# Kernel optimization log

Measured on AMD Instinct MI355X. Metric: run time of the kernel, lower is better.

The kernel has to match this reference:

```python
import jax, jax.numpy as jnp
import numpy as np

N_EMBED = 1024
N_HEADS = 16
HEAD_SIZE = N_EMBED // N_HEADS
BLOCK_SIZE = 256
LN_EPS = 1e-5


def _layernorm(x, g, b):
    mu = jnp.mean(x, axis=-1, keepdims=True)
    var = jnp.var(x, axis=-1, keepdims=True)
    return (x - mu) * jax.lax.rsqrt(var + LN_EPS) * g + b


def setup_inputs() -> dict:
    key = jax.random.key(0)
    ks = jax.random.split(key, 12)
    B, T, C, H, D = 64, 256, N_EMBED, N_HEADS, HEAD_SIZE
    s = lambda fan_in: 1.0 / np.sqrt(fan_in)
    return {
        "x": jax.random.normal(ks[0], (B, T, C), jnp.float32),
        # per-head Q/K/V projections (bias=False in torch), stacked over heads
        "Wq": jax.random.uniform(ks[1], (H, C, D), jnp.float32, -s(C), s(C)),
        "Wk": jax.random.uniform(ks[2], (H, C, D), jnp.float32, -s(C), s(C)),
        "Wv": jax.random.uniform(ks[3], (H, C, D), jnp.float32, -s(C), s(C)),
        "Wproj": jax.random.uniform(ks[4], (C, C), jnp.float32, -s(C), s(C)),
        "bproj": jax.random.uniform(ks[5], (C,), jnp.float32, -s(C), s(C)),
        "W1": jax.random.uniform(ks[6], (C, 4 * C), jnp.float32, -s(C), s(C)),
        "b1": jax.random.uniform(ks[7], (4 * C,), jnp.float32, -s(C), s(C)),
        "W2": jax.random.uniform(ks[8], (4 * C, C), jnp.float32, -s(4 * C), s(4 * C)),
        "b2": jax.random.uniform(ks[9], (C,), jnp.float32, -s(4 * C), s(4 * C)),
        "ln1_g": jnp.ones((C,), jnp.float32),
        "ln1_b": jnp.zeros((C,), jnp.float32),
        "ln2_g": jnp.ones((C,), jnp.float32),
        "ln2_b": jnp.zeros((C,), jnp.float32),
    }


def reference(x, Wq, Wk, Wv, Wproj, bproj, W1, b1, W2, b2, ln1_g, ln1_b, ln2_g, ln2_b):
    B, T, C = x.shape
    # --- self-attention sub-block ---
    h = _layernorm(x, ln1_g, ln1_b)
    q = jnp.einsum("btc,hcd->bhtd", h, Wq)
    k = jnp.einsum("btc,hcd->bhtd", h, Wk)
    v = jnp.einsum("btc,hcd->bhtd", h, Wv)
    # NOTE: original scales by C**-0.5 with C = n_embed (full dim), not head_size
    scores = jnp.einsum("bhtd,bhsd->bhts", q, k) * (C ** -0.5)
    causal = jnp.tril(jnp.ones((T, T), bool))
    scores = jnp.where(causal, scores, -jnp.inf)
    wei = jax.nn.softmax(scores, axis=-1)
    attn = jnp.einsum("bhts,bhsd->bhtd", wei, v)  # [B,H,T,D]
    attn = attn.transpose(0, 2, 1, 3).reshape(B, T, C)  # concat heads
    x = x + attn @ Wproj + bproj
    # --- feed-forward sub-block ---
    h2 = _layernorm(x, ln2_g, ln2_b)
    ffn = jax.nn.relu(h2 @ W1 + b1) @ W2 + b2
    return x + ffn
```

## Files before the change

### kernel.cpp

```cpp
#include <hip/hip_runtime.h>
#include <stdint.h>

using u16 = unsigned short;
using u32 = unsigned int;

typedef __attribute__((ext_vector_type(8))) short s16x8;
typedef __attribute__((ext_vector_type(4))) float f32x4;

__device__ __forceinline__ float bf2f(u16 u) { u32 t = (u32)u << 16; float f; __builtin_memcpy(&f, &t, 4); return f; }
__device__ __forceinline__ u16 f2bf(float f) {
  u32 u; __builtin_memcpy(&u, &f, 4);
  return (u16)((u + 0x7fffu + ((u >> 16) & 1u)) >> 16);
}

__device__ __forceinline__ void gload_lds16(const void* g, void* l) {
  __builtin_amdgcn_global_load_lds((const __attribute__((address_space(1))) void*)g,
                                   (__attribute__((address_space(3))) void*)l, 16, 0, 0);
}

__global__ __launch_bounds__(256)
void transpose_pack(const float* __restrict__ in, u16* __restrict__ out,
                    int R, int Cc, long in_bs, long out_bs)
{
  __shared__ float tile[32][33];
  in  += (size_t)blockIdx.z * in_bs;
  out += (size_t)blockIdx.z * out_bs;
  const int r0 = blockIdx.x * 32, c0 = blockIdx.y * 32;
  const int tx = threadIdx.x & 31, ty = threadIdx.x >> 5;
#pragma unroll
  for (int i = 0; i < 4; ++i) {
    int r = ty + i * 8;
    tile[r][tx] = in[(size_t)(r0 + r) * Cc + c0 + tx];
  }
  __syncthreads();
#pragma unroll
  for (int i = 0; i < 4; ++i) {
    int c = ty + i * 8;
    out[(size_t)(c0 + c) * R + r0 + tx] = f2bf(tile[tx][c]);
  }
}

template <int IN>
__global__ __launch_bounds__(256)
void ln_to_bf16(const void* __restrict__ xv, const float* __restrict__ g,
                const float* __restrict__ bta, u16* __restrict__ out)
{
  const int row = blockIdx.x, tid = threadIdx.x;
  float4 v;
  if constexpr (IN == 0) {
    v = ((const float4*)((const float*)xv + (size_t)row * 1024))[tid];
  } else {
    uint2 u = ((const uint2*)((const u16*)xv + (size_t)row * 1024))[tid];
    v.x = bf2f((u16)(u.x & 0xffff)); v.y = bf2f((u16)(u.x >> 16));
    v.z = bf2f((u16)(u.y & 0xffff)); v.w = bf2f((u16)(u.y >> 16));
  }
  float s  = v.x + v.y + v.z + v.w;
  float ss = v.x * v.x + v.y * v.y + v.z * v.z + v.w * v.w;
#pragma unroll
  for (int m = 1; m < 64; m <<= 1) {
    s  += __shfl_xor(s, m);
    ss += __shfl_xor(ss, m);
  }
  __shared__ float red[8];
  const int wave = tid >> 6, lane = tid & 63;
  if (lane == 0) { red[wave] = s; red[4 + wave] = ss; }
  __syncthreads();
  s  = red[0] + red[1] + red[2] + red[3];
  ss = red[4] + red[5] + red[6] + red[7];
  const float mu  = s * (1.f / 1024.f);
  const float var = ss * (1.f / 1024.f) - mu * mu;
  const float rs  = rsqrtf(var + 1e-5f);
  const float4 gg = ((const float4*)g)[tid];
  const float4 bb = ((const float4*)bta)[tid];
  u32 w0 = (u32)f2bf((v.x - mu) * rs * gg.x + bb.x) | ((u32)f2bf((v.y - mu) * rs * gg.y + bb.y) << 16);
  u32 w1 = (u32)f2bf((v.z - mu) * rs * gg.z + bb.z) | ((u32)f2bf((v.w - mu) * rs * gg.w + bb.w) << 16);
  u32* outp = (u32*)(out + (size_t)row * 1024 + tid * 4);
  outp[0] = w0; outp[1] = w1;
}

#define DSR(d, a, o) asm volatile("ds_read_b128 %0, %1 offset:" o : "=v"(d) : "v"(a))
#define ISSUE12(aR, bR) \
  DSR(bv0, bR, "0"); DSR(bv1, bR, "2048"); DSR(bv2, bR, "4096"); DSR(bv3, bR, "6144"); \
  DSR(av0, aR, "0"); DSR(av1, aR, "2048"); DSR(av2, aR, "4096"); DSR(av3, aR, "6144"); \
  DSR(av4, aR, "8192"); DSR(av5, aR, "10240"); DSR(av6, aR, "12288"); DSR(av7, aR, "14336")
#define MM(m, n) acc[m][n] = __builtin_amdgcn_mfma_f32_16x16x32_bf16(av##m, bv##n, acc[m][n], 0, 0, 0)
#define RUNG(m, cnt) \
  asm volatile("s_waitcnt lgkmcnt(" #cnt ")" ::: "memory"); \
  __builtin_amdgcn_sched_barrier(0); \
  MM(m, 0); MM(m, 1); MM(m, 2); MM(m, 3)
#define LADDER() \
  RUNG(0, 7); RUNG(1, 6); RUNG(2, 5); RUNG(3, 4); \
  RUNG(4, 3); RUNG(5, 2); RUNG(6, 1); RUNG(7, 0)

template <int EPI>
__device__ __forceinline__ void gemm_epilogue(f32x4 (&acc)[8][4], void* Cv, const float* bias,
                                              const void* resid, int N, int bm, int bn,
                                              int wr, int wc, int r, int kg)
{
#pragma unroll
  for (int m = 0; m < 8; ++m) {
#pragma unroll
    for (int n = 0; n < 4; ++n) {
#pragma unroll
      for (int j = 0; j < 4; ++j) {
        int row = bm * 256 + wr * 128 + m * 16 + kg * 4 + j;
        int col = bn * 256 + wc * 64 + n * 16 + r;
        size_t idx = (size_t)row * N + col;
        float v = acc[m][n][j];
        if constexpr (EPI == 0) {
          ((u16*)Cv)[idx] = f2bf(v);
        } else if constexpr (EPI == 1) {
          ((u16*)Cv)[idx] = f2bf(v + bias[col] + ((const float*)resid)[idx]);
        } else if constexpr (EPI == 2) {
          ((u16*)Cv)[idx] = f2bf(fmaxf(v + bias[col], 0.f));
        } else {
          ((float*)Cv)[idx] = v + bias[col] + bf2f(((const u16*)resid)[idx]);
        }
      }
    }
  }
}

template <int EPI>
__global__ __launch_bounds__(512, 2)
void gemm8p(const u16* __restrict__ A, const u16* __restrict__ B, void* __restrict__ Cv,
            const float* __restrict__ bias, const void* __restrict__ resid,
            int M, int N, int K, int CM, int CN, int XN)
{
  __shared__ u16 lds[65536];
  const int NT = K >> 6;
  const int tid = threadIdx.x;
  const int lane = tid & 63, wv = tid >> 6;
  const int wr = wv >> 2, wc = wv & 3;
  const int r = lane & 15, kg = lane >> 4;

  const int bid = blockIdx.x;
  const int x = bid & 7, i = bid >> 3;
  const int bm = (x / XN) * CM + i / CN;
  const int bn = (x % XN) * CN + i % CN;

  const u16* Ab = A + (size_t)bm * 256 * K;
  const u16* Bb = B + (size_t)bn * 256 * K;

  const u32 ldsb = (u32)(uintptr_t)lds;
  const u32 segb = (u32)((kg ^ (r >> 1)) << 4);
  const u32 abase = ldsb + (u32)((wr * 128 + r) * 128) + segb;
  const u32 bbase = ldsb + 65536u + (u32)((wc * 64 + r) * 128) + segb;

  f32x4 acc[8][4];
#pragma unroll
  for (int m = 0; m < 8; ++m)
#pragma unroll
    for (int n = 0; n < 4; ++n) acc[m][n] = f32x4{0.f, 0.f, 0.f, 0.f};

  auto stage = [&](const u16* src, int u, int h, int base_u16) {
#pragma unroll
    for (int jj = 0; jj < 2; ++jj) {
      int ci = jj * 512 + tid;
      int rl = ci >> 3;
      int sseg = (ci & 7) ^ ((rl >> 1) & 7);
      gload_lds16(src + (size_t)(h * 128 + rl) * K + u * 64 + sseg * 8,
                  &lds[base_u16 + h * 8192 + ci * 8]);
    }
  };

  stage(Ab, 0, 0, 0);      stage(Ab, 0, 1, 0);
  stage(Bb, 0, 0, 32768);  stage(Bb, 0, 1, 32768);
  asm volatile("s_waitcnt vmcnt(0)" ::: "memory");
  __builtin_amdgcn_s_barrier();

  for (int t = 0; t < NT; ++t) {
    const int buf = t & 1;
    const bool s1 = (t + 1) < NT;
    const int nb = (buf ^ 1) * 16384;
    const u32 aA0 = abase + (u32)(buf * 32768);
    const u32 aB0 = bbase + (u32)(buf * 32768);

    if (s1) {
      stage(Ab, t + 1, 0, nb);           stage(Ab, t + 1, 1, nb);
      stage(Bb, t + 1, 0, 32768 + nb);   stage(Bb, t + 1, 1, 32768 + nb);
    }
    __builtin_amdgcn_sched_barrier(0);
    __builtin_amdgcn_s_setprio(1);
    {
      s16x8 av0, av1, av2, av3, av4, av5, av6, av7, bv0, bv1, bv2, bv3;
      ISSUE12(aA0, aB0);
      LADDER();
    }
    {
      s16x8 av0, av1, av2, av3, av4, av5, av6, av7, bv0, bv1, bv2, bv3;
      ISSUE12(aA0 ^ 64u, aB0 ^ 64u);
      LADDER();
    }
    __builtin_amdgcn_s_setprio(0);
    __builtin_amdgcn_sched_barrier(0);
    asm volatile("s_waitcnt vmcnt(0)" ::: "memory");
    __builtin_amdgcn_s_barrier();
  }
  gemm_epilogue<EPI>(acc, Cv, bias, resid, N, bm, bn, wr, wc, r, kg);
}

template <int EPI>
__global__ __launch_bounds__(512, 2)
void gemm1b(const u16* __restrict__ A, const u16* __restrict__ B, void* __restrict__ Cv,
            const float* __restrict__ bias, const void* __restrict__ resid,
            int M, int N, int K, int CM, int CN, int XN)
{
  __shared__ u16 lds[32768];
  const int NT = K >> 6;
  const int tid = threadIdx.x;
  const int lane = tid & 63, wv = tid >> 6;
  const int wr = wv >> 2, wc = wv & 3;
  const int r = lane & 15, kg = lane >> 4;

  const int bid = blockIdx.x;
  const int x = bid & 7, i = bid >> 3;
  const int bm = (x / XN) * CM + i / CN;
  const int bn = (x % XN) * CN + i % CN;

  const u16* Ab = A + (size_t)bm * 256 * K;
  const u16* Bb = B + (size_t)bn * 256 * K;

  const u32 ldsb = (u32)(uintptr_t)lds;
  const u32 segb = (u32)((kg ^ (r >> 1)) << 4);
  const u32 aA0 = ldsb + (u32)((wr * 128 + r) * 128) + segb;
  const u32 aB0 = ldsb + 32768u + (u32)((wc * 64 + r) * 128) + segb;

  f32x4 acc[8][4];
#pragma unroll
  for (int m = 0; m < 8; ++m)
#pragma unroll
    for (int n = 0; n < 4; ++n) acc[m][n] = f32x4{0.f, 0.f, 0.f, 0.f};

  auto stage = [&](const u16* src, int u, int h, int base_u16) {
#pragma unroll
    for (int jj = 0; jj < 2; ++jj) {
      int ci = jj * 512 + tid;
      int rl = ci >> 3;
      int sseg = (ci & 7) ^ ((rl >> 1) & 7);
      gload_lds16(src + (size_t)(h * 128 + rl) * K + u * 64 + sseg * 8,
                  &lds[base_u16 + h * 8192 + ci * 8]);
    }
  };

  stage(Ab, 0, 0, 0);      stage(Ab, 0, 1, 0);
  stage(Bb, 0, 0, 16384);  stage(Bb, 0, 1, 16384);
  asm volatile("s_waitcnt vmcnt(0)" ::: "memory");
  __builtin_amdgcn_s_barrier();

  for (int t = 0; t < NT; ++t) {
    const bool s1 = (t + 1) < NT;
    __builtin_amdgcn_s_setprio(1);
    {
      s16x8 av0, av1, av2, av3, av4, av5, av6, av7, bv0, bv1, bv2, bv3;
      ISSUE12(aA0, aB0);
      LADDER();
    }
    {
      s16x8 av0, av1, av2, av3, av4, av5, av6, av7, bv0, bv1, bv2, bv3;
      ISSUE12(aA0 ^ 64u, aB0 ^ 64u);
      RUNG(0, 7); RUNG(1, 6); RUNG(2, 5); RUNG(3, 4);
      asm volatile("s_waitcnt lgkmcnt(0)" ::: "memory");
      __builtin_amdgcn_sched_barrier(0);
      __builtin_amdgcn_s_setprio(0);
      __builtin_amdgcn_s_barrier();
      __builtin_amdgcn_sched_barrier(0);
      if (s1) {
        stage(Ab, t + 1, 0, 0);      stage(Ab, t + 1, 1, 0);
        stage(Bb, t + 1, 0, 16384);  stage(Bb, t + 1, 1, 16384);
      }
      __builtin_amdgcn_sched_barrier(0);
      __builtin_amdgcn_s_setprio(1);
      MM(4, 0); MM(4, 1); MM(4, 2); MM(4, 3);
      MM(5, 0); MM(5, 1); MM(5, 2); MM(5, 3);
      MM(6, 0); MM(6, 1); MM(6, 2); MM(6, 3);
      MM(7, 0); MM(7, 1); MM(7, 2); MM(7, 3);
    }
    __builtin_amdgcn_s_setprio(0);
    __builtin_amdgcn_sched_barrier(0);
    asm volatile("s_waitcnt vmcnt(0)" ::: "memory");
    __builtin_amdgcn_s_barrier();
  }
  gemm_epilogue<EPI>(acc, Cv, bias, resid, N, bm, bn, wr, wc, r, kg);
}

#undef DSR
#undef ISSUE12
#undef MM
#undef RUNG
#undef LADDER

__global__ __launch_bounds__(256)
void attn_mfma(const u16* __restrict__ qkv, u16* __restrict__ outc)
{
  const int bh = blockIdx.x, b = bh >> 4, h = bh & 15;
  const int tid = threadIdx.x;
  const int lane = tid & 63, w = tid >> 6;
  const int r = lane & 15, kg = lane >> 4;

  __shared__ u16 Ks[64 * 64];
  __shared__ u16 Vt[64 * 72];
  __shared__ u16 P[4][64 * 72];

  const u16* qbase = qkv + (size_t)(b * 256) * 3072 + h * 64;

  s16x8 qf[4][2];
#pragma unroll
  for (int m = 0; m < 4; ++m)
#pragma unroll
    for (int ks = 0; ks < 2; ++ks)
      qf[m][ks] = *(const s16x8*)(qbase + (size_t)(w * 64 + m * 16 + r) * 3072 + ks * 32 + kg * 8);

  f32x4 of[4][4];
  float mrun[4][4], lrun[4][4];
#pragma unroll
  for (int m = 0; m < 4; ++m) {
#pragma unroll
    for (int n = 0; n < 4; ++n) of[m][n] = f32x4{0.f, 0.f, 0.f, 0.f};
#pragma unroll
    for (int j = 0; j < 4; ++j) { mrun[m][j] = -1e30f; lrun[m][j] = 0.f; }
  }

  const float cexp = 0.03125f * 1.4426950408889634f;

  for (int kt = 0; kt < 4; ++kt) {
#pragma unroll
    for (int jj = 0; jj < 2; ++jj) {
      int ci = jj * 256 + tid;
      int key = ci >> 3, seg = ci & 7;
      int sseg = seg ^ (key & 7);
      gload_lds16(qkv + (size_t)(b * 256 + kt * 64 + key) * 3072 + 1024 + h * 64 + sseg * 8,
                  &Ks[ci * 8]);
    }
    {
      int row = tid >> 2, q = tid & 3;
      const u16* vg = qkv + (size_t)(b * 256 + kt * 64 + row) * 3072 + 2048 + h * 64 + q * 16;
      union { uint4 u[2]; u16 s[16]; } vv;
      vv.u[0] = *(const uint4*)vg;
      vv.u[1] = *(const uint4*)(vg + 8);
#pragma unroll
      for (int i = 0; i < 16; ++i)
        Vt[(q * 16 + i) * 72 + row] = vv.s[i];
    }
    __syncthreads();

    if (w >= kt) {
      f32x4 s[4][4];
#pragma unroll
      for (int m = 0; m < 4; ++m)
#pragma unroll
        for (int n = 0; n < 4; ++n) s[m][n] = f32x4{0.f, 0.f, 0.f, 0.f};
#pragma unroll
      for (int ks = 0; ks < 2; ++ks) {
        s16x8 kb[4];
#pragma unroll
        for (int n = 0; n < 4; ++n) {
          int row = n * 16 + r;
          int sseg = (ks * 4 + kg) ^ (row & 7);
          kb[n] = *(const s16x8*)&Ks[row * 64 + sseg * 8];
        }
#pragma unroll
        for (int m = 0; m < 4; ++m)
#pragma unroll
          for (int n = 0; n < 4; ++n)
            s[m][n] = __builtin_amdgcn_mfma_f32_16x16x32_bf16(qf[m][ks], kb[n], s[m][n], 0, 0, 0);
      }
      if (kt == w) {
#pragma unroll
        for (int m = 0; m < 4; ++m)
#pragma unroll
          for (int n = 0; n < 4; ++n)
#pragma unroll
            for (int j = 0; j < 4; ++j)
              if (n * 16 + r > m * 16 + kg * 4 + j) s[m][n][j] = -1e30f;
      }
#pragma unroll
      for (int m = 0; m < 4; ++m) {
        float rm[4], rsc[4], ls[4];
#pragma unroll
        for (int j = 0; j < 4; ++j) {
          rm[j] = fmaxf(fmaxf(s[m][0][j], s[m][1][j]), fmaxf(s[m][2][j], s[m][3][j]));
          rm[j] = fmaxf(rm[j], __shfl_xor(rm[j], 1));
          rm[j] = fmaxf(rm[j], __shfl_xor(rm[j], 2));
          rm[j] = fmaxf(rm[j], __shfl_xor(rm[j], 4));
          rm[j] = fmaxf(rm[j], __shfl_xor(rm[j], 8));
          float mnew = fmaxf(mrun[m][j], rm[j]);
          rsc[j] = exp2f((mrun[m][j] - mnew) * cexp);
          mrun[m][j] = mnew;
          ls[j] = 0.f;
        }
#pragma unroll
        for (int n = 0; n < 4; ++n)
#pragma unroll
          for (int j = 0; j < 4; ++j) {
            float p = exp2f((s[m][n][j] - mrun[m][j]) * cexp);
            ls[j] += p;
            P[w][(m * 16 + kg * 4 + j) * 72 + n * 16 + r] = f2bf(p);
          }
#pragma unroll
        for (int j = 0; j < 4; ++j) {
          ls[j] += __shfl_xor(ls[j], 1);
          ls[j] += __shfl_xor(ls[j], 2);
          ls[j] += __shfl_xor(ls[j], 4);
          ls[j] += __shfl_xor(ls[j], 8);
          lrun[m][j] = lrun[m][j] * rsc[j] + ls[j];
        }
#pragma unroll
        for (int n = 0; n < 4; ++n)
#pragma unroll
          for (int j = 0; j < 4; ++j)
            of[m][n][j] *= rsc[j];
      }
#pragma unroll
      for (int kk = 0; kk < 2; ++kk) {
        s16x8 pa[4], vb[4];
#pragma unroll
        for (int m = 0; m < 4; ++m)
          pa[m] = *(const s16x8*)&P[w][(m * 16 + r) * 72 + kk * 32 + kg * 8];
#pragma unroll
        for (int n = 0; n < 4; ++n)
          vb[n] = *(const s16x8*)&Vt[(n * 16 + r) * 72 + kk * 32 + kg * 8];
#pragma unroll
        for (int m = 0; m < 4; ++m)
#pragma unroll
          for (int n = 0; n < 4; ++n)
            of[m][n] = __builtin_amdgcn_mfma_f32_16x16x32_bf16(pa[m], vb[n], of[m][n], 0, 0, 0);
      }
    }
    __syncthreads();
  }

#pragma unroll
  for (int m = 0; m < 4; ++m) {
    float inv[4];
#pragma unroll
    for (int j = 0; j < 4; ++j) inv[j] = 1.f / lrun[m][j];
#pragma unroll
    for (int n = 0; n < 4; ++n)
#pragma unroll
      for (int j = 0; j < 4; ++j) {
        int row = b * 256 + w * 64 + m * 16 + kg * 4 + j;
        outc[(size_t)row * 1024 + h * 64 + n * 16 + r] = f2bf(of[m][n][j] * inv[j]);
      }
  }
}

extern "C" void kernel_launch(void* const* d_in, const int* in_sizes, int n_in,
                              void* d_out, int out_size, void* d_ws, size_t ws_size,
                              hipStream_t stream) {
  (void)in_sizes; (void)n_in; (void)out_size; (void)ws_size;
  const float* x     = (const float*)d_in[0];
  const float* Wq    = (const float*)d_in[1];
  const float* Wk    = (const float*)d_in[2];
  const float* Wv    = (const float*)d_in[3];
  const float* Wproj = (const float*)d_in[4];
  const float* bproj = (const float*)d_in[5];
  const float* W1    = (const float*)d_in[6];
  const float* b1    = (const float*)d_in[7];
  const float* W2    = (const float*)d_in[8];
  const float* b2    = (const float*)d_in[9];
  const float* ln1g  = (const float*)d_in[10];
  const float* ln1b  = (const float*)d_in[11];
  const float* ln2g  = (const float*)d_in[12];
  const float* ln2b  = (const float*)d_in[13];
  float* out = (float*)d_out;

  char* ws = (char*)d_ws;
  u16*   WqkvT  = (u16*)(ws + 0);
  u16*   WprojT = (u16*)(ws + 6291456);
  u16*   W1T    = (u16*)(ws + 8388608);
  u16*   W2T    = (u16*)(ws + 16777216);
  u16*   hb     = (u16*)(ws + 25165824);
  u16*   qkvb   = (u16*)(ws + 58720256);
  u16*   x2     = (u16*)(ws + 159383552);
  u16*   h2     = (u16*)(ws + 226492416);
  u16*   ffn1   = (u16*)(ws + 25165824);
  u16*   attnout = hb;

  const int M = 16384;

  transpose_pack<<<dim3(32, 2, 16), 256, 0, stream>>>(Wq, WqkvT,           1024, 64, 65536, 65536);
  transpose_pack<<<dim3(32, 2, 16), 256, 0, stream>>>(Wk, WqkvT + 1048576, 1024, 64, 65536, 65536);
  transpose_pack<<<dim3(32, 2, 16), 256, 0, stream>>>(Wv, WqkvT + 2097152, 1024, 64, 65536, 65536);
  transpose_pack<<<dim3(32, 32, 1), 256, 0, stream>>>(Wproj, WprojT, 1024, 1024, 0, 0);
  transpose_pack<<<dim3(32, 128, 1), 256, 0, stream>>>(W1, W1T, 1024, 4096, 0, 0);
  transpose_pack<<<dim3(128, 32, 1), 256, 0, stream>>>(W2, W2T, 4096, 1024, 0, 0);

  ln_to_bf16<0><<<M, 256, 0, stream>>>(x, ln1g, ln1b, hb);

  gemm8p<0><<<768, 512, 0, stream>>>(hb, WqkvT, qkvb, nullptr, nullptr, M, 3072, 1024, 16, 6, 2);

  attn_mfma<<<1024, 256, 0, stream>>>(qkvb, attnout);

  gemm8p<1><<<256, 512, 0, stream>>>(attnout, WprojT, x2, bproj, x, M, 1024, 1024, 8, 4, 1);

  ln_to_bf16<1><<<M, 256, 0, stream>>>(x2, ln2g, ln2b, h2);

  gemm1b<2><<<1024, 512, 0, stream>>>(h2, W1T, ffn1, b1, nullptr, M, 4096, 1024, 16, 8, 2);

  gemm1b<3><<<256, 512, 0, stream>>>(ffn1, W2T, out, b2, x2, M, 1024, 4096, 8, 4, 1);
}
```

Baseline: 611.4 us.

## Shrink FFN GEMM tiles to 128x128 with 256-thread blocks for more occupancy

Replaces the 256x256-tile, 512-thread FFN GEMM with a 128x128-tile, 256-thread variant that uses half the LDS and a smaller 4x4 accumulator per wave, launched with four times as many blocks. The goal is more resident blocks per CU and better load balance, so memory latency is hidden by other blocks rather than by large per-block tiles. In exchange, operand reuse per byte loaded drops, which raises global and LDS traffic per FLOP. The epilogue is inlined with the new tile indexing.

```diff
diff --git a/kernel.cpp b/kernel.cpp
--- a/kernel.cpp
+++ b/kernel.cpp
@@ -83,12 +83,15 @@
   DSR(bv0, bR, "0"); DSR(bv1, bR, "2048"); DSR(bv2, bR, "4096"); DSR(bv3, bR, "6144"); \
   DSR(av0, aR, "0"); DSR(av1, aR, "2048"); DSR(av2, aR, "4096"); DSR(av3, aR, "6144"); \
   DSR(av4, aR, "8192"); DSR(av5, aR, "10240"); DSR(av6, aR, "12288"); DSR(av7, aR, "14336")
+#define ISSUE8(aR, bR) \
+  DSR(bv0, bR, "0"); DSR(bv1, bR, "2048"); DSR(bv2, bR, "4096"); DSR(bv3, bR, "6144"); \
+  DSR(av0, aR, "0"); DSR(av1, aR, "2048"); DSR(av2, aR, "4096"); DSR(av3, aR, "6144")
 #define MM(m, n) acc[m][n] = __builtin_amdgcn_mfma_f32_16x16x32_bf16(av##m, bv##n, acc[m][n], 0, 0, 0)
 #define RUNG(m, cnt) \
   asm volatile("s_waitcnt lgkmcnt(" #cnt ")" ::: "memory"); \
   __builtin_amdgcn_sched_barrier(0); \
   MM(m, 0); MM(m, 1); MM(m, 2); MM(m, 3)
-#define LADDER() \
+#define LADDER12() \
   RUNG(0, 7); RUNG(1, 6); RUNG(2, 5); RUNG(3, 4); \
   RUNG(4, 3); RUNG(5, 2); RUNG(6, 1); RUNG(7, 0)
 
@@ -185,12 +188,12 @@
     {
       s16x8 av0, av1, av2, av3, av4, av5, av6, av7, bv0, bv1, bv2, bv3;
       ISSUE12(aA0, aB0);
-      LADDER();
+      LADDER12();
     }
     {
       s16x8 av0, av1, av2, av3, av4, av5, av6, av7, bv0, bv1, bv2, bv3;
       ISSUE12(aA0 ^ 64u, aB0 ^ 64u);
-      LADDER();
+      LADDER12();
     }
     __builtin_amdgcn_s_setprio(0);
     __builtin_amdgcn_sched_barrier(0);
@@ -201,16 +204,16 @@
 }
 
 template <int EPI>
-__global__ __launch_bounds__(512, 2)
-void gemm1b(const u16* __restrict__ A, const u16* __restrict__ B, void* __restrict__ Cv,
+__global__ __launch_bounds__(256, 4)
+void gemm1s(const u16* __restrict__ A, const u16* __restrict__ B, void* __restrict__ Cv,
             const float* __restrict__ bias, const void* __restrict__ resid,
             int M, int N, int K, int CM, int CN, int XN)
 {
-  __shared__ u16 lds[32768];
+  __shared__ u16 lds[16384];
   const int NT = K >> 6;
   const int tid = threadIdx.x;
   const int lane = tid & 63, wv = tid >> 6;
-  const int wr = wv >> 2, wc = wv & 3;
+  const int wr = wv >> 1, wc = wv & 1;
   const int r = lane & 15, kg = lane >> 4;
 
   const int bid = blockIdx.x;
@@ -218,33 +221,32 @@
   const int bm = (x / XN) * CM + i / CN;
   const int bn = (x % XN) * CN + i % CN;
 
-  const u16* Ab = A + (size_t)bm * 256 * K;
-  const u16* Bb = B + (size_t)bn * 256 * K;
+  const u16* Ab = A + (size_t)bm * 128 * K;
+  const u16* Bb = B + (size_t)bn * 128 * K;
 
   const u32 ldsb = (u32)(uintptr_t)lds;
   const u32 segb = (u32)((kg ^ (r >> 1)) << 4);
-  const u32 aA0 = ldsb + (u32)((wr * 128 + r) * 128) + segb;
-  const u32 aB0 = ldsb + 32768u + (u32)((wc * 64 + r) * 128) + segb;
-
-  f32x4 acc[8][4];
-#pragma unroll
-  for (int m = 0; m < 8; ++m)
+  const u32 aA0 = ldsb + (u32)((wr * 64 + r) * 128) + segb;
+  const u32 aB0 = ldsb + 16384u + (u32)((wc * 64 + r) * 128) + segb;
+
+  f32x4 acc[4][4];
+#pragma unroll
+  for (int m = 0; m < 4; ++m)
 #pragma unroll
     for (int n = 0; n < 4; ++n) acc[m][n] = f32x4{0.f, 0.f, 0.f, 0.f};
 
-  auto stage = [&](const u16* src, int u, int h, int base_u16) {
-#pragma unroll
-    for (int jj = 0; jj < 2; ++jj) {
-      int ci = jj * 512 + tid;
+  auto stage = [&](const u16* src, int u, int base_u16) {
+#pragma unroll
+    for (int jj = 0; jj < 4; ++jj) {
+      int ci = jj * 256 + tid;
       int rl = ci >> 3;
       int sseg = (ci & 7) ^ ((rl >> 1) & 7);
-      gload_lds16(src + (size_t)(h * 128 + rl) * K + u * 64 + sseg * 8,
-                  &lds[base_u16 + h * 8192 + ci * 8]);
+      gload_lds16(src + (size_t)rl * K + u * 64 + sseg * 8, &lds[base_u16 + ci * 8]);
     }
   };
 
-  stage(Ab, 0, 0, 0);      stage(Ab, 0, 1, 0);
-  stage(Bb, 0, 0, 16384);  stage(Bb, 0, 1, 16384);
+  stage(Ab, 0, 0);
+  stage(Bb, 0, 8192);
   asm volatile("s_waitcnt vmcnt(0)" ::: "memory");
   __builtin_amdgcn_s_barrier();
 
@@ -252,43 +254,63 @@
     const bool s1 = (t + 1) < NT;
     __builtin_amdgcn_s_setprio(1);
     {
-      s16x8 av0, av1, av2, av3, av4, av5, av6, av7, bv0, bv1, bv2, bv3;
-      ISSUE12(aA0, aB0);
-      LADDER();
+      s16x8 av0, av1, av2, av3, bv0, bv1, bv2, bv3;
+      ISSUE8(aA0, aB0);
+      RUNG(0, 3); RUNG(1, 2); RUNG(2, 1); RUNG(3, 0);
     }
     {
-      s16x8 av0, av1, av2, av3, av4, av5, av6, av7, bv0, bv1, bv2, bv3;
-      ISSUE12(aA0 ^ 64u, aB0 ^ 64u);
-      RUNG(0, 7); RUNG(1, 6); RUNG(2, 5); RUNG(3, 4);
+      s16x8 av0, av1, av2, av3, bv0, bv1, bv2, bv3;
+      ISSUE8(aA0 ^ 64u, aB0 ^ 64u);
+      RUNG(0, 3); RUNG(1, 2); RUNG(2, 1);
       asm volatile("s_waitcnt lgkmcnt(0)" ::: "memory");
       __builtin_amdgcn_sched_barrier(0);
       __builtin_amdgcn_s_setprio(0);
       __builtin_amdgcn_s_barrier();
       __builtin_amdgcn_sched_barrier(0);
       if (s1) {
-        stage(Ab, t + 1, 0, 0);      stage(Ab, t + 1, 1, 0);
-        stage(Bb, t + 1, 0, 16384);  stage(Bb, t + 1, 1, 16384);
+        stage(Ab, t + 1, 0);
+        stage(Bb, t + 1, 8192);
       }
       __builtin_amdgcn_sched_barrier(0);
       __builtin_amdgcn_s_setprio(1);
-      MM(4, 0); MM(4, 1); MM(4, 2); MM(4, 3);
-      MM(5, 0); MM(5, 1); MM(5, 2); MM(5, 3);
-      MM(6, 0); MM(6, 1); MM(6, 2); MM(6, 3);
-      MM(7, 0); MM(7, 1); MM(7, 2); MM(7, 3);
+      MM(3, 0); MM(3, 1); MM(3, 2); MM(3, 3);
     }
     __builtin_amdgcn_s_setprio(0);
     __builtin_amdgcn_sched_barrier(0);
     asm volatile("s_waitcnt vmcnt(0)" ::: "memory");
     __builtin_amdgcn_s_barrier();
   }
-  gemm_epilogue<EPI>(acc, Cv, bias, resid, N, bm, bn, wr, wc, r, kg);
+
+#pragma unroll
+  for (int m = 0; m < 4; ++m) {
+#pragma unroll
+    for (int n = 0; n < 4; ++n) {
+#pragma unroll
+      for (int j = 0; j < 4; ++j) {
+        int row = bm * 128 + wr * 64 + m * 16 + kg * 4 + j;
+        int col = bn * 128 + wc * 64 + n * 16 + r;
+        size_t idx = (size_t)row * N + col;
+        float v = acc[m][n][j];
+        if constexpr (EPI == 0) {
+          ((u16*)Cv)[idx] = f2bf(v);
+        } else if constexpr (EPI == 1) {
+          ((u16*)Cv)[idx] = f2bf(v + bias[col] + ((const float*)resid)[idx]);
+        } else if constexpr (EPI == 2) {
+          ((u16*)Cv)[idx] = f2bf(fmaxf(v + bias[col], 0.f));
+        } else {
+          ((float*)Cv)[idx] = v + bias[col] + bf2f(((const u16*)resid)[idx]);
+        }
+      }
+    }
+  }
 }
 
 #undef DSR
 #undef ISSUE12
+#undef ISSUE8
 #undef MM
 #undef RUNG
-#undef LADDER
+#undef LADDER12
 
 __global__ __launch_bounds__(256)
 void attn_mfma(const u16* __restrict__ qkv, u16* __restrict__ outc)
@@ -496,7 +518,7 @@
 
   ln_to_bf16<1><<<M, 256, 0, stream>>>(x2, ln2g, ln2b, h2);
 
-  gemm1b<2><<<1024, 512, 0, stream>>>(h2, W1T, ffn1, b1, nullptr, M, 4096, 1024, 16, 8, 2);
-
-  gemm1b<3><<<256, 512, 0, stream>>>(ffn1, W2T, out, b2, x2, M, 1024, 4096, 8, 4, 1);
-}
+  gemm1s<2><<<4096, 256, 0, stream>>>(h2, W1T, ffn1, b1, nullptr, M, 4096, 1024, 64, 8, 4);
+
+  gemm1s<3><<<1024, 256, 0, stream>>>(ffn1, W2T, out, b2, x2, M, 1024, 4096, 16, 8, 1);
+}
```

Measured after the change: 568.2 us. -7.1%, faster.
